# Performance work log

Hardware: AMD Instinct MI355X
Metric: run time of the kernel (lower is better)

The kernel has to match this reference:

```python
import jax, jax.numpy as jnp
import numpy as np

N_NODES = 50000
N_EDGES = 800000
NODE_NF = 128
HIDDEN_NF = 256
LN_EPS = 1e-5


def _layernorm(x, gamma, beta):
    mu = jnp.mean(x, axis=-1, keepdims=True)
    var = jnp.mean((x - mu) ** 2, axis=-1, keepdims=True)
    return (x - mu) * jax.lax.rsqrt(var + LN_EPS) * gamma + beta


def setup_inputs() -> dict:
    key = jax.random.key(0)
    ks = jax.random.split(key, 8)
    h = jax.random.normal(ks[0], (N_NODES, NODE_NF), dtype=jnp.float32)
    edge_index = jax.random.randint(ks[1], (2, N_EDGES), 0, N_NODES, dtype=jnp.int32)
    # edge_mlp: Linear(2*node_nf -> hidden), LayerNorm(hidden), SiLU, Linear(hidden -> hidden)
    s1 = 1.0 / np.sqrt(2 * NODE_NF)
    W1 = jax.random.uniform(ks[2], (2 * NODE_NF, HIDDEN_NF), jnp.float32, -s1, s1)
    b1 = jnp.zeros((HIDDEN_NF,), jnp.float32)
    g1 = jnp.ones((HIDDEN_NF,), jnp.float32)
    be1 = jnp.zeros((HIDDEN_NF,), jnp.float32)
    s2 = 1.0 / np.sqrt(HIDDEN_NF)
    W2 = jax.random.uniform(ks[3], (HIDDEN_NF, HIDDEN_NF), jnp.float32, -s2, s2)
    b2 = jnp.zeros((HIDDEN_NF,), jnp.float32)
    # node_mlp: Linear(node_nf+hidden -> hidden), LayerNorm(hidden), SiLU, Linear(hidden -> node_nf)
    s3 = 1.0 / np.sqrt(NODE_NF + HIDDEN_NF)
    W3 = jax.random.uniform(ks[4], (NODE_NF + HIDDEN_NF, HIDDEN_NF), jnp.float32, -s3, s3)
    b3 = jnp.zeros((HIDDEN_NF,), jnp.float32)
    g2 = jnp.ones((HIDDEN_NF,), jnp.float32)
    be2 = jnp.zeros((HIDDEN_NF,), jnp.float32)
    W4 = jax.random.uniform(ks[5], (HIDDEN_NF, NODE_NF), jnp.float32, -s2, s2)
    b4 = jnp.zeros((NODE_NF,), jnp.float32)
    return {"h": h, "edge_index": edge_index,
            "W1": W1, "b1": b1, "g1": g1, "be1": be1, "W2": W2, "b2": b2,
            "W3": W3, "b3": b3, "g2": g2, "be2": be2, "W4": W4, "b4": b4}


def reference(h, edge_index, W1, b1, g1, be1, W2, b2, W3, b3, g2, be2, W4, b4):
    row, col = edge_index[0], edge_index[1]
    # message: gather source/target node features, edge MLP
    src = h[row]                      # [E, node_nf]
    tgt = h[col]                      # [E, node_nf]
    e_in = jnp.concatenate([src, tgt], axis=1)          # [E, 2*node_nf]
    m = _layernorm(e_in @ W1 + b1, g1, be1)
    m = jax.nn.silu(m) @ W2 + b2                        # [E, hidden]
    # aggregate: scatter-sum messages to row nodes, node MLP, residual
    agg = jax.ops.segment_sum(m, row, num_segments=h.shape[0])  # [N, hidden]
    n_in = jnp.concatenate([h, agg], axis=1)            # [N, node_nf+hidden]
    dh = _layernorm(n_in @ W3 + b3, g2, be2)
    dh = jax.nn.silu(dh) @ W4 + b4                      # [N, node_nf]
    return h + dh
```

## Files before the change

kernel.cpp:

```cpp
#include <hip/hip_runtime.h>
#include <hip/hip_bf16.h>
#include <stdint.h>

#define NNODES 50000
#define NEDGES 800000
#define NF 128
#define NH 256

typedef __attribute__((ext_vector_type(8))) __bf16 bf16x8;
typedef __attribute__((ext_vector_type(8))) unsigned short u16x8;
typedef __attribute__((ext_vector_type(4))) float f32x4;

__device__ __forceinline__ unsigned short f2bf(float f) {
    union { float f; unsigned int u; } v; v.f = f;
    unsigned int r = v.u + 0x7fffu + ((v.u >> 16) & 1u);
    return (unsigned short)(r >> 16);
}

__device__ __forceinline__ void gload16(const void* g, void* l) {
    __builtin_amdgcn_global_load_lds(
        (const __attribute__((address_space(1))) void*)g,
        (__attribute__((address_space(3))) void*)l,
        16, 0, 0);
}

__global__ __launch_bounds__(256) void tcvt_kernel(const float* __restrict__ W,
                                                   unsigned short* __restrict__ Wt, int K, int Nn) {
    int i = blockIdx.x * 256 + threadIdx.x;
    if (i < K * Nn) {
        int k = i / Nn, n = i - k * Nn;
        Wt[n * K + k] = f2bf(W[i]);
    }
}

__global__ __launch_bounds__(256) void wpq_kernel(const float* __restrict__ W1,
                                                  unsigned short* __restrict__ Wtpq) {
    int i = blockIdx.x * 256 + threadIdx.x;
    if (i < 512 * 128) {
        int n = i >> 7, k = i & 127;
        float v = (n < 256) ? W1[k * 256 + n] : W1[(128 + k) * 256 + (n - 256)];
        Wtpq[i] = f2bf(v);
    }
}

__global__ __launch_bounds__(256) void hist_kernel(const int* __restrict__ row, int* __restrict__ cnt) {
    int e = blockIdx.x * 256 + threadIdx.x;
    if (e < NEDGES) atomicAdd(&cnt[row[e]], 1);
}

__global__ __launch_bounds__(1024) void scan_kernel(const int* __restrict__ cnt, int* __restrict__ base, int n) {
    __shared__ int wsum[16];
    __shared__ int s_carry;
    const int tid = threadIdx.x;
    const int lane = tid & 63;
    const int wv = tid >> 6;
    if (tid == 0) s_carry = 0;
    __syncthreads();
    for (int off = 0; off < n; off += 1024) {
        int v = (off + tid < n) ? cnt[off + tid] : 0;
        int acc = v;
        #pragma unroll
        for (int s = 1; s < 64; s <<= 1) {
            int t = __shfl_up(acc, s);
            if (lane >= s) acc += t;
        }
        if (lane == 63) wsum[wv] = acc;
        __syncthreads();
        if (wv == 0) {
            int x = (lane < 16) ? wsum[lane] : 0;
            #pragma unroll
            for (int s = 1; s < 16; s <<= 1) {
                int t = __shfl_up(x, s);
                if (lane >= s) x += t;
            }
            if (lane < 16) wsum[lane] = x;
        }
        __syncthreads();
        int c = s_carry;
        int wtot = __shfl(acc, 63);
        int woff = wsum[wv] - wtot;
        if (off + tid < n) base[off + tid] = c + woff + acc - v;
        __syncthreads();
        if (tid == 0) s_carry = c + wsum[15];
        __syncthreads();
    }
}

__global__ __launch_bounds__(256) void scatter_kernel(const int* __restrict__ ei,
                                                      const int* __restrict__ base,
                                                      int* __restrict__ cursor,
                                                      unsigned short* __restrict__ ssrc,
                                                      unsigned short* __restrict__ sdst) {
    int e = blockIdx.x * 256 + threadIdx.x;
    if (e < NEDGES) {
        int r = ei[e];
        int c = ei[NEDGES + e];
        int pos = base[r] + atomicAdd(&cursor[r], 1);
        ssrc[pos] = (unsigned short)r;
        sdst[pos] = (unsigned short)c;
    }
}

__global__ __launch_bounds__(256, 2)
void pq_kernel(const float* __restrict__ h,
               const unsigned short* __restrict__ Wtpq,
               const float* __restrict__ b1,
               unsigned short* __restrict__ P,
               unsigned short* __restrict__ Q)
{
    __shared__ __align__(16) unsigned short A_lds[64 * 128];
    const int tid = threadIdx.x;
    const int lane = tid & 63;
    const int w = tid >> 6;
    const int l15 = lane & 15;
    const int g = lane >> 4;
    const int r0 = blockIdx.x * 64;

    float b1r[4];
    #pragma unroll
    for (int n = 0; n < 4; ++n) b1r[n] = b1[w * 64 + n * 16 + l15];

    #pragma unroll
    for (int i = 0; i < 4; ++i) {
        int idx = i * 256 + tid;
        int row = idx >> 4, cl = idx & 15;
        int nd = r0 + row; if (nd >= NNODES) nd = NNODES - 1;
        const float* sp = h + (size_t)nd * NF + ((cl ^ (row & 7)) * 8);
        float4 va = *(const float4*)sp;
        float4 vb = *(const float4*)(sp + 4);
        u16x8 mv;
        mv[0] = f2bf(va.x); mv[1] = f2bf(va.y); mv[2] = f2bf(va.z); mv[3] = f2bf(va.w);
        mv[4] = f2bf(vb.x); mv[5] = f2bf(vb.y); mv[6] = f2bf(vb.z); mv[7] = f2bf(vb.w);
        *(u16x8*)(void*)&A_lds[row * 128 + cl * 8] = mv;
    }
    __syncthreads();

    #pragma unroll
    for (int p = 0; p < 2; ++p) {
        bf16x8 Bf[4][4];
        #pragma unroll
        for (int n = 0; n < 4; ++n) {
            int cn = w * 64 + n * 16 + l15;
            #pragma unroll
            for (int ks = 0; ks < 4; ++ks)
                Bf[n][ks] = *(const bf16x8*)(const void*)&Wtpq[(size_t)(p * 256 + cn) * 128 + ks * 32 + 8 * g];
        }
        f32x4 acc[4][4] = {};
        #pragma unroll
        for (int ks = 0; ks < 4; ++ks) {
            bf16x8 af[4];
            #pragma unroll
            for (int m = 0; m < 4; ++m) {
                int r = m * 16 + l15;
                af[m] = *(const bf16x8*)(const void*)&A_lds[r * 128 + ((ks * 32 + 8 * g) ^ ((r & 7) << 3))];
            }
            #pragma unroll
            for (int m = 0; m < 4; ++m)
                #pragma unroll
                for (int n = 0; n < 4; ++n)
                    acc[m][n] = __builtin_amdgcn_mfma_f32_16x16x32_bf16(af[m], Bf[n][ks], acc[m][n], 0, 0, 0);
        }
        unsigned short* dst = p ? Q : P;
        #pragma unroll
        for (int m = 0; m < 4; ++m)
            #pragma unroll
            for (int rr = 0; rr < 4; ++rr) {
                int row = m * 16 + 4 * g + rr;
                int nd = r0 + row;
                if (nd < NNODES) {
                    #pragma unroll
                    for (int n = 0; n < 4; ++n) {
                        int col = w * 64 + n * 16 + l15;
                        float v = acc[m][n][rr] + (p ? 0.f : b1r[n]);
                        dst[(size_t)nd * NH + col] = f2bf(v);
                    }
                }
            }
    }
}

__global__ __launch_bounds__(256, 3)
void edge_kernel(const unsigned short* __restrict__ P,
                 const unsigned short* __restrict__ Q,
                 const unsigned short* __restrict__ ssrc,
                 const unsigned short* __restrict__ sdst,
                 const unsigned short* __restrict__ Wt2,
                 const float* __restrict__ g1, const float* __restrict__ be1,
                 const float* __restrict__ b2,
                 float* __restrict__ agg)
{
    __shared__ __align__(16) char smem[33280];
    unsigned short* M_lds = (unsigned short*)smem;
    float* S = (float*)smem;
    float (*s_part)[64][2] = (float(*)[64][2])(void*)smem;
    __shared__ unsigned short s_src[64];
    __shared__ float s_mr[64][2];
    __shared__ float s_g1[256], s_be1[256];

    const int tid = threadIdx.x;
    const int lane = tid & 63;
    const int w = tid >> 6;
    const int l15 = lane & 15;
    const int g = lane >> 4;
    const int e0 = blockIdx.x * 64;
    const int r = lane;

    s_g1[tid] = g1[tid]; s_be1[tid] = be1[tid];
    if (tid < 64) s_src[tid] = ssrc[e0 + tid];

    float b2r[4];
    #pragma unroll
    for (int n = 0; n < 4; ++n) b2r[n] = b2[w * 64 + n * 16 + l15];

    int nds = ssrc[e0 + r];
    int ndt = sdst[e0 + r];
    const bf16x8* Pp = (const bf16x8*)(const void*)(P + (size_t)nds * NH + w * 64);
    const bf16x8* Qp = (const bf16x8*)(const void*)(Q + (size_t)ndt * NH + w * 64);

    u16x8 xb[8];
    float sum = 0.f, sq = 0.f;
    #pragma unroll
    for (int j = 0; j < 8; ++j) {
        bf16x8 pv = Pp[j];
        bf16x8 qv = Qp[j];
        u16x8 mv;
        #pragma unroll
        for (int k = 0; k < 8; ++k) {
            float xx = (float)pv[k] + (float)qv[k];
            sum += xx;
            sq += xx * xx;
            mv[k] = f2bf(xx);
        }
        xb[j] = mv;
    }
    s_part[w][r][0] = sum;
    s_part[w][r][1] = sq;
    __syncthreads();
    if (tid < 64) {
        float s = s_part[0][tid][0] + s_part[1][tid][0] + s_part[2][tid][0] + s_part[3][tid][0];
        float q = s_part[0][tid][1] + s_part[1][tid][1] + s_part[2][tid][1] + s_part[3][tid][1];
        float mean = s * (1.f / 256.f);
        float var = q * (1.f / 256.f) - mean * mean;
        s_mr[tid][0] = mean;
        s_mr[tid][1] = rsqrtf(var + 1e-5f);
    }
    __syncthreads();

    {
        float mean = s_mr[r][0], rstd = s_mr[r][1];
        #pragma unroll
        for (int j = 0; j < 8; ++j) {
            bf16x8 xv = *(bf16x8*)(void*)&xb[j];
            u16x8 mv;
            #pragma unroll
            for (int k = 0; k < 8; ++k) {
                int col = w * 64 + j * 8 + k;
                float y = ((float)xv[k] - mean) * rstd * s_g1[col] + s_be1[col];
                float sy = y * (1.f / (1.f + __expf(-y)));
                mv[k] = f2bf(sy);
            }
            *(u16x8*)(void*)&M_lds[r * 256 + w * 64 + ((j ^ (r & 7)) * 8)] = mv;
        }
    }
    __syncthreads();

    f32x4 acc2[4][4] = {};
    #pragma unroll
    for (int ks = 0; ks < 8; ++ks) {
        bf16x8 bfr[4];
        #pragma unroll
        for (int n = 0; n < 4; ++n) {
            int cn = w * 64 + n * 16 + l15;
            bfr[n] = *(const bf16x8*)(const void*)&Wt2[cn * 256 + ks * 32 + 8 * g];
        }
        bf16x8 af[4];
        #pragma unroll
        for (int m = 0; m < 4; ++m) {
            int rr_ = m * 16 + l15;
            af[m] = *(const bf16x8*)(const void*)&M_lds[rr_ * 256 + ((ks * 32 + 8 * g) ^ ((rr_ & 7) << 3))];
        }
        #pragma unroll
        for (int m = 0; m < 4; ++m)
            #pragma unroll
            for (int n = 0; n < 4; ++n)
                acc2[m][n] = __builtin_amdgcn_mfma_f32_16x16x32_bf16(af[m], bfr[n], acc2[m][n], 0, 0, 0);
    }
    __syncthreads();

    {
        const int col = tid;
        float run = 0.f;
        int prev = s_src[0];
        #pragma unroll
        for (int p = 0; p < 2; ++p) {
            #pragma unroll
            for (int mm = 0; mm < 2; ++mm) {
                int m = 2 * p + mm;
                #pragma unroll
                for (int rr = 0; rr < 4; ++rr) {
                    int lrow = mm * 16 + 4 * g + rr;
                    #pragma unroll
                    for (int n = 0; n < 4; ++n) {
                        int c2 = w * 64 + n * 16 + l15;
                        S[lrow * 260 + c2] = acc2[m][n][rr] + b2r[n];
                    }
                }
            }
            __syncthreads();
            #pragma unroll 1
            for (int rr = 0; rr < 32; ++rr) {
                int nd = s_src[32 * p + rr];
                if (nd != prev) {
                    atomicAdd(&agg[(size_t)prev * NH + col], run);
                    run = 0.f;
                    prev = nd;
                }
                run += S[rr * 260 + col];
            }
            if (p == 0) __syncthreads();
        }
        atomicAdd(&agg[(size_t)prev * NH + col], run);
    }
}

__global__ __launch_bounds__(256, 2)
void node_kernel(const float* __restrict__ h,
                 const float* __restrict__ agg,
                 const unsigned short* __restrict__ Wt3,
                 const unsigned short* __restrict__ Wt4,
                 const float* __restrict__ b3, const float* __restrict__ g2,
                 const float* __restrict__ be2, const float* __restrict__ b4,
                 float* __restrict__ out)
{
    __shared__ __align__(16) unsigned short A_lds[64 * 64];
    __shared__ __align__(16) unsigned short B_lds[256 * 64];
    __shared__ __align__(16) unsigned short M_lds[64 * 256];
    __shared__ float s_mr[64][2];
    __shared__ float s_b3[256], s_g2[256], s_be2[256], s_b4[128];

    const int tid = threadIdx.x;
    const int lane = tid & 63;
    const int w = tid >> 6;
    const int l15 = lane & 15;
    const int g = lane >> 4;
    const int r0 = blockIdx.x * 64;

    s_b3[tid] = b3[tid]; s_g2[tid] = g2[tid]; s_be2[tid] = be2[tid];
    if (tid < 128) s_b4[tid] = b4[tid];
    __syncthreads();

    f32x4 acc[4][4] = {};

    for (int kt = 0; kt < 6; ++kt) {
        #pragma unroll
        for (int i = 0; i < 8; ++i) {
            int c = i * 256 + w * 64 + lane;
            int n = c >> 3, kbl = c & 7;
            int kb = kbl ^ (n & 7);
            const unsigned short* src = Wt3 + n * 384 + kt * 64 + kb * 8;
            gload16(src, &B_lds[(i * 256 + w * 64) * 8]);
        }
        #pragma unroll
        for (int i = 0; i < 2; ++i) {
            int idx = i * 256 + tid;
            int row = idx >> 3, cl = idx & 7;
            int nd = r0 + row; if (nd >= NNODES) nd = NNODES - 1;
            int scol = (cl ^ (row & 7)) * 8;
            const float* sp = (kt < 2) ? (h + (size_t)nd * NF + kt * 64 + scol)
                                       : (agg + (size_t)nd * NH + (kt - 2) * 64 + scol);
            float4 va = *(const float4*)sp;
            float4 vb = *(const float4*)(sp + 4);
            u16x8 mv;
            mv[0] = f2bf(va.x); mv[1] = f2bf(va.y); mv[2] = f2bf(va.z); mv[3] = f2bf(va.w);
            mv[4] = f2bf(vb.x); mv[5] = f2bf(vb.y); mv[6] = f2bf(vb.z); mv[7] = f2bf(vb.w);
            *(u16x8*)(void*)&A_lds[row * 64 + cl * 8] = mv;
        }
        __syncthreads();
        #pragma unroll
        for (int kk = 0; kk < 2; ++kk) {
            int ke = kk * 32 + 8 * g;
            bf16x8 af[4], bfr[4];
            #pragma unroll
            for (int m = 0; m < 4; ++m) {
                int rr_ = m * 16 + l15;
                af[m] = *(const bf16x8*)(const void*)&A_lds[rr_ * 64 + (ke ^ ((rr_ & 7) << 3))];
            }
            #pragma unroll
            for (int n = 0; n < 4; ++n) {
                int cn = w * 64 + n * 16 + l15;
                bfr[n] = *(const bf16x8*)(const void*)&B_lds[cn * 64 + (ke ^ ((cn & 7) << 3))];
            }
            #pragma unroll
            for (int m = 0; m < 4; ++m)
                #pragma unroll
                for (int n = 0; n < 4; ++n)
                    acc[m][n] = __builtin_amdgcn_mfma_f32_16x16x32_bf16(af[m], bfr[n], acc[m][n], 0, 0, 0);
        }
        __syncthreads();
    }

    float psum[4][4], psq[4][4];
    #pragma unroll
    for (int m = 0; m < 4; ++m)
        #pragma unroll
        for (int rr = 0; rr < 4; ++rr) { psum[m][rr] = 0.f; psq[m][rr] = 0.f; }
    #pragma unroll
    for (int m = 0; m < 4; ++m)
        #pragma unroll
        for (int n = 0; n < 4; ++n) {
            int col = w * 64 + n * 16 + l15;
            float bb = s_b3[col];
            #pragma unroll
            for (int rr = 0; rr < 4; ++rr) {
                float xv = acc[m][n][rr] + bb;
                acc[m][n][rr] = xv;
                psum[m][rr] += xv;
                psq[m][rr] += xv * xv;
            }
        }
    #pragma unroll
    for (int m = 0; m < 4; ++m)
        #pragma unroll
        for (int rr = 0; rr < 4; ++rr) {
            float s = psum[m][rr], q = psq[m][rr];
            s += __shfl_xor(s, 1); s += __shfl_xor(s, 2); s += __shfl_xor(s, 4); s += __shfl_xor(s, 8);
            q += __shfl_xor(q, 1); q += __shfl_xor(q, 2); q += __shfl_xor(q, 4); q += __shfl_xor(q, 8);
            psum[m][rr] = s; psq[m][rr] = q;
        }
    float vs = 0.f, vq = 0.f;
    #pragma unroll
    for (int m = 0; m < 4; ++m)
        #pragma unroll
        for (int rr = 0; rr < 4; ++rr) {
            bool sel = (l15 == m * 4 + rr);
            vs = sel ? psum[m][rr] : vs;
            vq = sel ? psq[m][rr] : vq;
        }
    float (*s_part)[64][2] = (float(*)[64][2])(void*)M_lds;
    {
        int row = (l15 >> 2) * 16 + 4 * g + (l15 & 3);
        s_part[w][row][0] = vs;
        s_part[w][row][1] = vq;
    }
    __syncthreads();
    if (tid < 64) {
        float s = s_part[0][tid][0] + s_part[1][tid][0] + s_part[2][tid][0] + s_part[3][tid][0];
        float q = s_part[0][tid][1] + s_part[1][tid][1] + s_part[2][tid][1] + s_part[3][tid][1];
        float mean = s * (1.f / 256.f);
        float var = q * (1.f / 256.f) - mean * mean;
        s_mr[tid][0] = mean;
        s_mr[tid][1] = rsqrtf(var + 1e-5f);
    }
    __syncthreads();

    #pragma unroll
    for (int m = 0; m < 4; ++m)
        #pragma unroll
        for (int rr = 0; rr < 4; ++rr) {
            int row = m * 16 + 4 * g + rr;
            float mean = s_mr[row][0], rstd = s_mr[row][1];
            #pragma unroll
            for (int n = 0; n < 4; ++n) {
                int col = w * 64 + n * 16 + l15;
                float y = (acc[m][n][rr] - mean) * rstd * s_g2[col] + s_be2[col];
                float sy = y * (1.f / (1.f + __expf(-y)));
                M_lds[row * 256 + (col ^ ((row & 7) << 3))] = f2bf(sy);
            }
        }
    __syncthreads();

    f32x4 acc4[4][2] = {};
    for (int kt = 0; kt < 4; ++kt) {
        #pragma unroll
        for (int i = 0; i < 4; ++i) {
            int c = i * 256 + w * 64 + lane;
            int n = c >> 3, kbl = c & 7;
            int kb = kbl ^ (n & 7);
            const unsigned short* src = Wt4 + n * 256 + kt * 64 + kb * 8;
            gload16(src, &B_lds[(i * 256 + w * 64) * 8]);
        }
        __syncthreads();
        #pragma unroll
        for (int kk = 0; kk < 2; ++kk) {
            int keB = kk * 32 + 8 * g;
            int keA = kt * 64 + keB;
            bf16x8 af[4], bfr[2];
            #pragma unroll
            for (int m = 0; m < 4; ++m) {
                int rr_ = m * 16 + l15;
                af[m] = *(const bf16x8*)(const void*)&M_lds[rr_ * 256 + (keA ^ ((rr_ & 7) << 3))];
            }
            #pragma unroll
            for (int n2 = 0; n2 < 2; ++n2) {
                int cn = w * 32 + n2 * 16 + l15;
                bfr[n2] = *(const bf16x8*)(const void*)&B_lds[cn * 64 + (keB ^ ((cn & 7) << 3))];
            }
            #pragma unroll
            for (int m = 0; m < 4; ++m)
                #pragma unroll
                for (int n2 = 0; n2 < 2; ++n2)
                    acc4[m][n2] = __builtin_amdgcn_mfma_f32_16x16x32_bf16(af[m], bfr[n2], acc4[m][n2], 0, 0, 0);
        }
        __syncthreads();
    }

    #pragma unroll
    for (int m = 0; m < 4; ++m)
        #pragma unroll
        for (int rr = 0; rr < 4; ++rr) {
            int row = m * 16 + 4 * g + rr;
            int nd = r0 + row;
            if (nd < NNODES) {
                #pragma unroll
                for (int n2 = 0; n2 < 2; ++n2) {
                    int col = w * 32 + n2 * 16 + l15;
                    out[(size_t)nd * NF + col] = h[(size_t)nd * NF + col] + acc4[m][n2][rr] + s_b4[col];
                }
            }
        }
}

extern "C" void kernel_launch(void* const* d_in, const int* in_sizes, int n_in,
                              void* d_out, int out_size, void* d_ws, size_t ws_size,
                              hipStream_t stream) {
    const float* h   = (const float*)d_in[0];
    const int* ei    = (const int*)d_in[1];
    const float* W1  = (const float*)d_in[2];
    const float* b1  = (const float*)d_in[3];
    const float* g1  = (const float*)d_in[4];
    const float* be1 = (const float*)d_in[5];
    const float* W2  = (const float*)d_in[6];
    const float* b2  = (const float*)d_in[7];
    const float* W3  = (const float*)d_in[8];
    const float* b3  = (const float*)d_in[9];
    const float* g2  = (const float*)d_in[10];
    const float* be2 = (const float*)d_in[11];
    const float* W4  = (const float*)d_in[12];
    const float* b4  = (const float*)d_in[13];
    float* out = (float*)d_out;

    char* ws = (char*)d_ws;
    float* agg            = (float*)(ws);
    int* cnt              = (int*)(ws);
    int* basep            = (int*)(ws + 200000);
    int* cursor           = (int*)(ws + 400000);
    unsigned short* P     = (unsigned short*)(ws + 51200000);
    unsigned short* Q     = (unsigned short*)d_out;
    unsigned short* ssrc  = (unsigned short*)(ws + 76800000);
    unsigned short* sdst  = (unsigned short*)(ws + 78400000);
    unsigned short* Wtpq  = (unsigned short*)(ws + 80000000);
    unsigned short* Wt2   = (unsigned short*)(ws + 80131072);
    unsigned short* Wt3   = (unsigned short*)(ws + 80262144);
    unsigned short* Wt4   = (unsigned short*)(ws + 80458752);

    hipMemsetAsync(ws, 0, 600000, stream);

    wpq_kernel<<<(512 * 128 + 255) / 256, 256, 0, stream>>>(W1, Wtpq);
    tcvt_kernel<<<(256 * 256 + 255) / 256, 256, 0, stream>>>(W2, Wt2, 256, 256);
    tcvt_kernel<<<(384 * 256 + 255) / 256, 256, 0, stream>>>(W3, Wt3, 384, 256);
    tcvt_kernel<<<(256 * 128 + 255) / 256, 256, 0, stream>>>(W4, Wt4, 256, 128);

    hist_kernel<<<(NEDGES + 255) / 256, 256, 0, stream>>>(ei, cnt);
    scan_kernel<<<1, 1024, 0, stream>>>(cnt, basep, NNODES);
    scatter_kernel<<<(NEDGES + 255) / 256, 256, 0, stream>>>(ei, basep, cursor, ssrc, sdst);

    pq_kernel<<<(NNODES + 63) / 64, 256, 0, stream>>>(h, Wtpq, b1, P, Q);

    hipMemsetAsync(agg, 0, (size_t)NNODES * NH * sizeof(float), stream);

    edge_kernel<<<NEDGES / 64, 256, 0, stream>>>(P, Q, ssrc, sdst, Wt2, g1, be1, b2, agg);
    node_kernel<<<(NNODES + 63) / 64, 256, 0, stream>>>(h, agg, Wt3, Wt4, b3, g2, be2, b4, out);
}
```

Baseline: 574.7 us.

## Read node-MLP weights straight from global memory and drop an edge-kernel barrier

In the node kernel, the weight tiles for W3 and W4 are no longer staged into LDS. The MFMA B fragments are now read directly from global memory (L2-cached), which frees 32KB of LDS and allows raising the occupancy hint to 3 blocks per CU. The second-GEMM loop also loses its barriers. In the edge kernel, every lane now computes the LayerNorm mean and rstd itself, removing one __syncthreads. Gamma and beta are loaded as vectors, and the b2 load is deferred to cut register pressure. The risk is higher global/L2 traffic and latency on the weight loads with no LDS reuse.

New measurement: 531.6 us (median of 2 runs). 7.5% less time.

```diff
diff --git a/kernel.cpp b/kernel.cpp
--- a/kernel.cpp
+++ b/kernel.cpp
@@ -192,10 +192,9 @@
     __shared__ __align__(16) char smem[33280];
     unsigned short* M_lds = (unsigned short*)smem;
     float* S = (float*)smem;
-    float (*s_part)[64][2] = (float(*)[64][2])(void*)smem;
+    __shared__ float s_part[4][64][2];
     __shared__ unsigned short s_src[64];
-    __shared__ float s_mr[64][2];
-    __shared__ float s_g1[256], s_be1[256];
+    __shared__ __align__(16) float s_g1[256], s_be1[256];
 
     const int tid = threadIdx.x;
     const int lane = tid & 63;
@@ -208,10 +207,6 @@
     s_g1[tid] = g1[tid]; s_be1[tid] = be1[tid];
     if (tid < 64) s_src[tid] = ssrc[e0 + tid];
 
-    float b2r[4];
-    #pragma unroll
-    for (int n = 0; n < 4; ++n) b2r[n] = b2[w * 64 + n * 16 + l15];
-
     int nds = ssrc[e0 + r];
     int ndt = sdst[e0 + r];
     const bf16x8* Pp = (const bf16x8*)(const void*)(P + (size_t)nds * NH + w * 64);
@@ -236,26 +231,30 @@
     s_part[w][r][0] = sum;
     s_part[w][r][1] = sq;
     __syncthreads();
-    if (tid < 64) {
-        float s = s_part[0][tid][0] + s_part[1][tid][0] + s_part[2][tid][0] + s_part[3][tid][0];
-        float q = s_part[0][tid][1] + s_part[1][tid][1] + s_part[2][tid][1] + s_part[3][tid][1];
-        float mean = s * (1.f / 256.f);
+
+    float mean, rstd;
+    {
+        float s = s_part[0][r][0] + s_part[1][r][0] + s_part[2][r][0] + s_part[3][r][0];
+        float q = s_part[0][r][1] + s_part[1][r][1] + s_part[2][r][1] + s_part[3][r][1];
+        mean = s * (1.f / 256.f);
         float var = q * (1.f / 256.f) - mean * mean;
-        s_mr[tid][0] = mean;
-        s_mr[tid][1] = rsqrtf(var + 1e-5f);
-    }
-    __syncthreads();
+        rstd = rsqrtf(var + 1e-5f);
+    }
 
     {
-        float mean = s_mr[r][0], rstd = s_mr[r][1];
         #pragma unroll
         for (int j = 0; j < 8; ++j) {
             bf16x8 xv = *(bf16x8*)(void*)&xb[j];
+            float ga[8], bb[8];
+            *(float4*)&ga[0] = *(const float4*)&s_g1[w * 64 + j * 8];
+            *(float4*)&ga[4] = *(const float4*)&s_g1[w * 64 + j * 8 + 4];
+            *(float4*)&bb[0] = *(const float4*)&s_be1[w * 64 + j * 8];
+            *(float4*)&bb[4] = *(const float4*)&s_be1[w * 64 + j * 8 + 4];
             u16x8 mv;
             #pragma unroll
             for (int k = 0; k < 8; ++k) {
-                int col = w * 64 + j * 8 + k;
-                float y = ((float)xv[k] - mean) * rstd * s_g1[col] + s_be1[col];
+                float xx = (float)xv[k];
+                float y = (xx - mean) * rstd * ga[k] + bb[k];
                 float sy = y * (1.f / (1.f + __expf(-y)));
                 mv[k] = f2bf(sy);
             }
@@ -288,6 +287,10 @@
     __syncthreads();
 
     {
+        float b2r[4];
+        #pragma unroll
+        for (int n = 0; n < 4; ++n) b2r[n] = b2[w * 64 + n * 16 + l15];
+
         const int col = tid;
         float run = 0.f;
         int prev = s_src[0];
@@ -323,7 +326,7 @@
     }
 }
 
-__global__ __launch_bounds__(256, 2)
+__global__ __launch_bounds__(256, 3)
 void node_kernel(const float* __restrict__ h,
                  const float* __restrict__ agg,
                  const unsigned short* __restrict__ Wt3,
@@ -333,7 +336,6 @@
                  float* __restrict__ out)
 {
     __shared__ __align__(16) unsigned short A_lds[64 * 64];
-    __shared__ __align__(16) unsigned short B_lds[256 * 64];
     __shared__ __align__(16) unsigned short M_lds[64 * 256];
     __shared__ float s_mr[64][2];
     __shared__ float s_b3[256], s_g2[256], s_be2[256], s_b4[128];
@@ -352,14 +354,6 @@
     f32x4 acc[4][4] = {};
 
     for (int kt = 0; kt < 6; ++kt) {
-        #pragma unroll
-        for (int i = 0; i < 8; ++i) {
-            int c = i * 256 + w * 64 + lane;
-            int n = c >> 3, kbl = c & 7;
-            int kb = kbl ^ (n & 7);
-            const unsigned short* src = Wt3 + n * 384 + kt * 64 + kb * 8;
-            gload16(src, &B_lds[(i * 256 + w * 64) * 8]);
-        }
         #pragma unroll
         for (int i = 0; i < 2; ++i) {
             int idx = i * 256 + tid;
@@ -388,7 +382,7 @@
             #pragma unroll
             for (int n = 0; n < 4; ++n) {
                 int cn = w * 64 + n * 16 + l15;
-                bfr[n] = *(const bf16x8*)(const void*)&B_lds[cn * 64 + (ke ^ ((cn & 7) << 3))];
+                bfr[n] = *(const bf16x8*)(const void*)&Wt3[(size_t)cn * 384 + kt * 64 + ke];
             }
             #pragma unroll
             for (int m = 0; m < 4; ++m)
@@ -472,15 +466,6 @@
     f32x4 acc4[4][2] = {};
     for (int kt = 0; kt < 4; ++kt) {
         #pragma unroll
-        for (int i = 0; i < 4; ++i) {
-            int c = i * 256 + w * 64 + lane;
-            int n = c >> 3, kbl = c & 7;
-            int kb = kbl ^ (n & 7);
-            const unsigned short* src = Wt4 + n * 256 + kt * 64 + kb * 8;
-            gload16(src, &B_lds[(i * 256 + w * 64) * 8]);
-        }
-        __syncthreads();
-        #pragma unroll
         for (int kk = 0; kk < 2; ++kk) {
             int keB = kk * 32 + 8 * g;
             int keA = kt * 64 + keB;
@@ -493,7 +478,7 @@
             #pragma unroll
             for (int n2 = 0; n2 < 2; ++n2) {
                 int cn = w * 32 + n2 * 16 + l15;
-                bfr[n2] = *(const bf16x8*)(const void*)&B_lds[cn * 64 + (keB ^ ((cn & 7) << 3))];
+                bfr[n2] = *(const bf16x8*)(const void*)&Wt4[(size_t)cn * 256 + kt * 64 + keB];
             }
             #pragma unroll
             for (int m = 0; m < 4; ++m)
@@ -501,7 +486,6 @@
                 for (int n2 = 0; n2 < 2; ++n2)
                     acc4[m][n2] = __builtin_amdgcn_mfma_f32_16x16x32_bf16(af[m], bfr[n2], acc4[m][n2], 0, 0, 0);
         }
-        __syncthreads();
     }
 
     #pragma unroll
```
